# Optimization experiments

Hardware: AMD Instinct MI355X
Metric: run time of the kernel (lower is better)

## Reference

```python
import jax, jax.numpy as jnp
import numpy as np

LN_EPS = 1e-5


def _mlp(x, W1, b1, W2, b2, g, beta):
    # build_mlp_d: Linear -> ReLU -> Linear -> LayerNorm (mlp_layers=2, lay_norm=True)
    h = jax.nn.relu(x @ W1 + b1)
    h = h @ W2 + b2
    mu = jnp.mean(h, axis=-1, keepdims=True)
    var = jnp.var(h, axis=-1, keepdims=True)
    return (h - mu) * jax.lax.rsqrt(var + LN_EPS) * g + beta


def setup_inputs() -> dict:
    E, N, L, EIF = 524288, 65536, 128, 3
    key = jax.random.key(0)
    ks = iter(jax.random.split(key, 48))
    def rn(shape, s=1.0):
        return jax.random.normal(next(ks), shape, dtype=jnp.float32) * s
    inp = {}
    inp["edge_index"] = jax.random.randint(next(ks), (2, E), 0, N)
    inp["edge_dx_"] = rn((E, 3))
    inp["edge_attr"] = rn((E, EIF))
    for nm in ["vector_a", "vector_b", "vector_c",
               "senders_v_t_", "senders_v_tm1_", "senders_w_t_", "senders_w_tm1_",
               "senders_a_t_", "senders_alpha_t_",
               "receivers_v_t_", "receivers_v_tm1_", "receivers_w_t_", "receivers_w_tm1_",
               "receivers_a_t_", "receivers_alpha_t_"]:
        inp[nm] = rn((E, 3))
    inp["node_latent"] = rn((N, L))
    def mlp_params(pfx, din):
        inp[pfx + "_W1"] = rn((din, L), 0.05)
        inp[pfx + "_b1"] = jnp.zeros((L,), jnp.float32)
        inp[pfx + "_W2"] = rn((L, L), 0.05)
        inp[pfx + "_b2"] = jnp.zeros((L,), jnp.float32)
        inp[pfx + "_g"] = jnp.ones((L,), jnp.float32)
        inp[pfx + "_beta"] = jnp.zeros((L,), jnp.float32)
    mlp_params("fe", 18)        # edge_feat_encoder
    mlp_params("ee", 1 + EIF)   # edge_encoder
    mlp_params("ie", 3 * L)     # interaction_encoder
    return inp


def reference(edge_index, edge_dx_, edge_attr, vector_a, vector_b, vector_c,
              senders_v_t_, senders_v_tm1_, senders_w_t_, senders_w_tm1_,
              senders_a_t_, senders_alpha_t_,
              receivers_v_t_, receivers_v_tm1_, receivers_w_t_, receivers_w_tm1_,
              receivers_a_t_, receivers_alpha_t_,
              node_latent,
              fe_W1, fe_b1, fe_W2, fe_b2, fe_g, fe_beta,
              ee_W1, ee_b1, ee_W2, ee_b2, ee_g, ee_beta,
              ie_W1, ie_b1, ie_W2, ie_b2, ie_g, ie_beta):
    senders, receivers = edge_index[0], edge_index[1]
    basis = jnp.stack([vector_a, vector_b, vector_c], axis=1)  # [E,3,3]
    # Fuse the 12 small bmm projections into two batched einsums.
    s_stack = jnp.stack([senders_v_t_, senders_v_tm1_, senders_w_t_, senders_w_tm1_,
                         senders_a_t_, senders_alpha_t_], axis=1)   # [E,6,3]
    r_stack = jnp.stack([receivers_v_t_, receivers_v_tm1_, receivers_w_t_, receivers_w_tm1_,
                         receivers_a_t_, receivers_alpha_t_], axis=1)
    s_proj = jnp.einsum('eij,ekj->eki', basis, s_stack)  # [E,6,3]
    r_proj = jnp.einsum('eij,ekj->eki', basis, r_stack)
    # signs: -v_t, -v_tm1, -w_t, +w_tm1, -a_t, +alpha_t (receivers side)
    r_sign = jnp.array([-1.0, -1.0, -1.0, 1.0, -1.0, 1.0], jnp.float32)[None, :, None]
    E = s_proj.shape[0]
    senders_features = s_proj.reshape(E, 18)
    receivers_features = (r_proj * r_sign).reshape(E, 18)
    edge_dx_norm = jnp.linalg.norm(edge_dx_, axis=1, keepdims=True)  # [E,1]
    edge_latent = _mlp(jnp.concatenate([edge_dx_norm, edge_attr], axis=1),
                       ee_W1, ee_b1, ee_W2, ee_b2, ee_g, ee_beta)
    senders_latent = _mlp(senders_features, fe_W1, fe_b1, fe_W2, fe_b2, fe_g, fe_beta)
    receivers_latent = _mlp(receivers_features, fe_W1, fe_b1, fe_W2, fe_b2, fe_g, fe_beta)
    node_sum = node_latent[senders] + node_latent[receivers]  # [E,L]
    msg_input = jnp.concatenate([senders_latent + receivers_latent, node_sum, edge_latent], axis=1)
    return _mlp(msg_input, ie_W1, ie_b1, ie_W2, ie_b2, ie_g, ie_beta)
```

## Files before the change

### kernel.cpp

```cpp
#include <hip/hip_runtime.h>

typedef __attribute__((ext_vector_type(4))) float fx4;
typedef __attribute__((ext_vector_type(8))) unsigned short u16x8;
typedef __attribute__((ext_vector_type(8))) __bf16 bf16x8;

static __device__ __forceinline__ unsigned short f2bf(float f) {
  unsigned int u = __builtin_bit_cast(unsigned int, f);
  u += 0x7fffu + ((u >> 16) & 1u);
  return (unsigned short)(u >> 16);
}
static __device__ __forceinline__ fx4 mfma16(u16x8 a, u16x8 b, fx4 c) {
  return __builtin_amdgcn_mfma_f32_16x16x32_bf16(
      __builtin_bit_cast(bf16x8, a), __builtin_bit_cast(bf16x8, b), c, 0, 0, 0);
}

static __device__ __forceinline__ int swz128(int row, int col) {
  return row * 128 + (col ^ ((row & 7) << 3));
}
static __device__ __forceinline__ int swz32(int row, int col) {
  return row * 32 + (col ^ (((row >> 1) & 3) << 3));
}

#define WT_FE1 0
#define WT_FE2 4096
#define WT_EE1 20480
#define WT_EE2 24576
#define WT_A   40960
#define WT_B   57344
#define WT_C   73728
#define WT_IE2 90112
#define WT_TOTAL 106496

__global__ void prep_weights(const float* __restrict__ feW1, const float* __restrict__ feW2,
                             const float* __restrict__ eeW1, const float* __restrict__ eeW2,
                             const float* __restrict__ ieW1, const float* __restrict__ ieW2,
                             unsigned short* __restrict__ wt) {
  int i = blockIdx.x * 256 + threadIdx.x;
  if (i >= WT_TOTAL) return;
  int base, n, k, kpad;
  float val;
  if (i < WT_FE2)      { base = WT_FE1; n = i >> 5; k = i & 31; kpad = 32;
                         val = (k < 18) ? feW1[k * 128 + n] : 0.f; }
  else if (i < WT_EE1) { base = WT_FE2; int j = i - WT_FE2; n = j >> 7; k = j & 127; kpad = 128;
                         val = feW2[k * 128 + n]; }
  else if (i < WT_EE2) { base = WT_EE1; int j = i - WT_EE1; n = j >> 5; k = j & 31; kpad = 32;
                         val = (k < 4) ? eeW1[k * 128 + n] : 0.f; }
  else if (i < WT_A)   { base = WT_EE2; int j = i - WT_EE2; n = j >> 7; k = j & 127; kpad = 128;
                         val = eeW2[k * 128 + n]; }
  else if (i < WT_B)   { base = WT_A;   int j = i - WT_A;   n = j >> 7; k = j & 127; kpad = 128;
                         val = ieW1[k * 128 + n]; }
  else if (i < WT_C)   { base = WT_B;   int j = i - WT_B;   n = j >> 7; k = j & 127; kpad = 128;
                         val = ieW1[(128 + k) * 128 + n]; }
  else if (i < WT_IE2) { base = WT_C;   int j = i - WT_C;   n = j >> 7; k = j & 127; kpad = 128;
                         val = ieW1[(256 + k) * 128 + n]; }
  else                 { base = WT_IE2; int j = i - WT_IE2; n = j >> 7; k = j & 127; kpad = 128;
                         val = ieW2[k * 128 + n]; }
  int dst = (kpad == 32) ? base + n * 32 + (k ^ (((n >> 1) & 3) << 3))
                         : base + n * 128 + (k ^ ((n & 7) << 3));
  wt[dst] = f2bf(val);
}

template<int KPAD, int KT>
static __device__ __forceinline__ void gemm_lds(const unsigned short* As,
                                                const unsigned short* Ws,
                                                fx4* acc, int l16, int lgr) {
#pragma unroll
  for (int kk = 0; kk < KT; kk++) {
    const int k0 = kk * 32 + lgr * 8;
    u16x8 af = *(const u16x8*)(As + ((KPAD == 32) ? swz32(l16, k0) : swz128(l16, k0)));
#pragma unroll
    for (int nt = 0; nt < 8; nt++) {
      const int n = nt * 16 + l16;
      u16x8 bf = *(const u16x8*)(Ws + ((KPAD == 32) ? swz32(n, k0) : swz128(n, k0)));
      acc[nt] = mfma16(af, bf, acc[nt]);
    }
  }
}

static __device__ __forceinline__ void relu_store(fx4* acc, const float* __restrict__ bias,
                                                  unsigned short* dst, int l16, int lgr) {
#pragma unroll
  for (int nt = 0; nt < 8; nt++) {
    const int col = nt * 16 + l16;
    const float b = bias[col];
#pragma unroll
    for (int r = 0; r < 4; r++) {
      float v = acc[nt][r] + b;
      dst[swz128(lgr * 4 + r, col)] = f2bf(v > 0.f ? v : 0.f);
    }
  }
}

static __device__ __forceinline__ void ln_rows(fx4* acc, const float* __restrict__ bias, int l16) {
  float sum[4] = {0, 0, 0, 0}, sq[4] = {0, 0, 0, 0};
#pragma unroll
  for (int nt = 0; nt < 8; nt++) {
    const float b = bias[nt * 16 + l16];
#pragma unroll
    for (int r = 0; r < 4; r++) {
      float v = acc[nt][r] + b; acc[nt][r] = v;
      sum[r] += v; sq[r] += v * v;
    }
  }
#pragma unroll
  for (int r = 0; r < 4; r++) {
    float s_ = sum[r], q_ = sq[r];
#pragma unroll
    for (int m = 1; m < 16; m <<= 1) { s_ += __shfl_xor(s_, m, 64); q_ += __shfl_xor(q_, m, 64); }
    const float mu = s_ * (1.f / 128.f);
    const float rs = rsqrtf(q_ * (1.f / 128.f) - mu * mu + 1e-5f);
#pragma unroll
    for (int nt = 0; nt < 8; nt++) acc[nt][r] = (acc[nt][r] - mu) * rs;
  }
}

struct ParamsFE {
  const float* basis[3];
  const float* sv[6]; const float* rv[6];
  const float* b1; const float* b2; const float* g; const float* be;
  const unsigned short* wt;
  unsigned short* msg;
  int ntiles;
};

__global__ __launch_bounds__(512) void fe_kernel(ParamsFE p) {
  extern __shared__ unsigned short lds[];
  const int tid = threadIdx.x;
  const int wave = tid >> 6, lane = tid & 63;
  const int l16 = lane & 15, lgr = lane >> 4;
#pragma unroll
  for (int i = tid * 8; i < 20480; i += 4096)
    *(u16x8*)(lds + i) = *(const u16x8*)(p.wt + WT_FE1 + i);
  const unsigned short* W1 = lds;
  const unsigned short* W2 = lds + 4096;
  unsigned short* h1 = lds + 20480 + wave * 2560;
  unsigned short* feat = h1 + 2048;
  __syncthreads();
#pragma unroll
  for (int j = 0; j < 4; j++) { int c = 18 + lgr * 4 + j; if (c < 32) feat[swz32(l16, c)] = 0; }
  const fx4 z4 = {0.f, 0.f, 0.f, 0.f};

  for (int t = blockIdx.x; t < p.ntiles; t += gridDim.x) {
    const int e0 = t * 128 + wave * 16;
    const size_t e = (size_t)(e0 + l16);
    float bx[3][3];
#pragma unroll
    for (int i = 0; i < 3; i++) {
      const float* bp = p.basis[i] + 3 * e;
      bx[i][0] = bp[0]; bx[i][1] = bp[1]; bx[i][2] = bp[2];
    }
    fx4 latS[8];
#pragma unroll
    for (int side = 0; side < 2; side++) {
      const bool isR = (side == 1);
#pragma unroll
      for (int k = 0; k < 6; k++) {
        if ((k & 3) == lgr) {
          const float* vp = (isR ? p.rv[k] : p.sv[k]) + 3 * e;
          const float v0 = vp[0], v1 = vp[1], v2 = vp[2];
          const float sgn = (isR && k != 3 && k != 5) ? -1.f : 1.f;
#pragma unroll
          for (int i = 0; i < 3; i++) {
            float d = (bx[i][0] * v0 + bx[i][1] * v1 + bx[i][2] * v2) * sgn;
            feat[swz32(l16, k * 3 + i)] = f2bf(d);
          }
        }
      }
      fx4 acc[8];
#pragma unroll
      for (int b = 0; b < 8; b++) acc[b] = z4;
      gemm_lds<32, 1>(feat, W1, acc, l16, lgr);
      relu_store(acc, p.b1, h1, l16, lgr);
#pragma unroll
      for (int b = 0; b < 8; b++) acc[b] = z4;
      gemm_lds<128, 4>(h1, W2, acc, l16, lgr);
      ln_rows(acc, p.b2, l16);
      if (!isR) {
#pragma unroll
        for (int nt = 0; nt < 8; nt++) {
          const int col = nt * 16 + l16;
          const float gg = p.g[col], bb = p.be[col];
#pragma unroll
          for (int r = 0; r < 4; r++) latS[nt][r] = acc[nt][r] * gg + bb;
        }
      } else {
#pragma unroll
        for (int nt = 0; nt < 8; nt++) {
          const int col = nt * 16 + l16;
          const float gg = p.g[col], bb = p.be[col];
#pragma unroll
          for (int r = 0; r < 4; r++)
            p.msg[(size_t)(e0 + lgr * 4 + r) * 256 + col] =
                f2bf(latS[nt][r] + acc[nt][r] * gg + bb);
        }
      }
    }
  }
}

struct ParamsEE {
  const float* dx; const float* attr;
  const float* b1; const float* b2; const float* g; const float* be;
  const unsigned short* wt;
  unsigned short* msg;
  int ntiles;
};

__global__ __launch_bounds__(512) void ee_kernel(ParamsEE p) {
  extern __shared__ unsigned short lds[];
  const int tid = threadIdx.x;
  const int wave = tid >> 6, lane = tid & 63;
  const int l16 = lane & 15, lgr = lane >> 4;
#pragma unroll
  for (int i = tid * 8; i < 20480; i += 4096)
    *(u16x8*)(lds + i) = *(const u16x8*)(p.wt + WT_EE1 + i);
  const unsigned short* W1 = lds;
  const unsigned short* W2 = lds + 4096;
  unsigned short* h1 = lds + 20480 + wave * 2560;
  unsigned short* feat = h1 + 2048;
  __syncthreads();
#pragma unroll
  for (int j = 0; j < 7; j++) feat[swz32(l16, 4 + lgr * 7 + j)] = 0;
  const fx4 z4 = {0.f, 0.f, 0.f, 0.f};

  for (int t = blockIdx.x; t < p.ntiles; t += gridDim.x) {
    const int e0 = t * 128 + wave * 16;
    const size_t e = (size_t)(e0 + l16);
    if (lgr == 0) {
      float d0 = p.dx[3 * e], d1 = p.dx[3 * e + 1], d2 = p.dx[3 * e + 2];
      feat[swz32(l16, 0)] = f2bf(sqrtf(d0 * d0 + d1 * d1 + d2 * d2));
    } else {
      feat[swz32(l16, lgr)] = f2bf(p.attr[3 * e + (lgr - 1)]);
    }
    fx4 acc[8];
#pragma unroll
    for (int b = 0; b < 8; b++) acc[b] = z4;
    gemm_lds<32, 1>(feat, W1, acc, l16, lgr);
    relu_store(acc, p.b1, h1, l16, lgr);
#pragma unroll
    for (int b = 0; b < 8; b++) acc[b] = z4;
    gemm_lds<128, 4>(h1, W2, acc, l16, lgr);
    ln_rows(acc, p.b2, l16);
#pragma unroll
    for (int nt = 0; nt < 8; nt++) {
      const int col = nt * 16 + l16;
      const float gg = p.g[col], bb = p.be[col];
#pragma unroll
      for (int r = 0; r < 4; r++)
        p.msg[(size_t)(e0 + lgr * 4 + r) * 256 + 128 + col] =
            f2bf(acc[nt][r] * gg + bb);
    }
  }
}

struct ParamsIE {
  const int* eidx;
  const float* nl;
  const float* b1; const float* b2; const float* g; const float* be;
  const unsigned short* wt;
  const unsigned short* msg;
  float* out;
  int E; int ntiles;
};

__global__ __launch_bounds__(512) void ie_kernel(ParamsIE p) {
  extern __shared__ unsigned short dyn[];
  const int tid = threadIdx.x;
  const int wave = tid >> 6, lane = tid & 63;
  const int l16 = lane & 15, lgr = lane >> 4;
#pragma unroll
  for (int i = tid * 8; i < 49152; i += 4096)
    *(u16x8*)(dyn + i) = *(const u16x8*)(p.wt + WT_A + i);
  const unsigned short* WA = dyn;
  const unsigned short* WB = dyn + 16384;
  const unsigned short* WC = dyn + 32768;
  unsigned short* h1 = dyn + 49152 + wave * 2048;
  __syncthreads();
  const fx4 z4 = {0.f, 0.f, 0.f, 0.f};

  for (int t = blockIdx.x; t < p.ntiles; t += gridDim.x) {
    const int e0 = t * 128 + wave * 16;
    const size_t e = (size_t)(e0 + l16);
    const int sidx = p.eidx[e];
    const int ridx = p.eidx[(size_t)p.E + e];
    const unsigned short* mrow = p.msg + e * 256;
    const float* ns = p.nl + (size_t)sidx * 128;
    const float* nr = p.nl + (size_t)ridx * 128;
    fx4 acc[8];
#pragma unroll
    for (int b = 0; b < 8; b++) acc[b] = z4;
#pragma unroll
    for (int c = 0; c < 4; c++) {
      const int k0 = c * 32 + lgr * 8;
      fx4 a0 = *(const fx4*)(ns + k0), a1 = *(const fx4*)(ns + k0 + 4);
      fx4 b0 = *(const fx4*)(nr + k0), b1 = *(const fx4*)(nr + k0 + 4);
      u16x8 af;
#pragma unroll
      for (int j = 0; j < 4; j++) { af[j] = f2bf(a0[j] + b0[j]); af[4 + j] = f2bf(a1[j] + b1[j]); }
#pragma unroll
      for (int nt = 0; nt < 8; nt++) {
        u16x8 bf = *(const u16x8*)(WB + swz128(nt * 16 + l16, k0));
        acc[nt] = mfma16(af, bf, acc[nt]);
      }
    }
#pragma unroll
    for (int c = 0; c < 4; c++) {
      const int k0 = c * 32 + lgr * 8;
      u16x8 af = *(const u16x8*)(mrow + k0);
#pragma unroll
      for (int nt = 0; nt < 8; nt++) {
        u16x8 bf = *(const u16x8*)(WA + swz128(nt * 16 + l16, k0));
        acc[nt] = mfma16(af, bf, acc[nt]);
      }
    }
#pragma unroll
    for (int c = 0; c < 4; c++) {
      const int k0 = c * 32 + lgr * 8;
      u16x8 af = *(const u16x8*)(mrow + 128 + k0);
#pragma unroll
      for (int nt = 0; nt < 8; nt++) {
        u16x8 bf = *(const u16x8*)(WC + swz128(nt * 16 + l16, k0));
        acc[nt] = mfma16(af, bf, acc[nt]);
      }
    }
    relu_store(acc, p.b1, h1, l16, lgr);
#pragma unroll
    for (int b = 0; b < 8; b++) acc[b] = z4;
    gemm_lds<128, 4>(h1, p.wt + WT_IE2, acc, l16, lgr);
    ln_rows(acc, p.b2, l16);
#pragma unroll
    for (int nt = 0; nt < 8; nt++) {
      const int col = nt * 16 + l16;
      const float gg = p.g[col], bb = p.be[col];
#pragma unroll
      for (int r = 0; r < 4; r++)
        p.out[(size_t)(e0 + lgr * 4 + r) * 128 + col] = acc[nt][r] * gg + bb;
    }
  }
}

extern "C" void kernel_launch(void* const* d_in, const int* in_sizes, int n_in,
                              void* d_out, int out_size, void* d_ws, size_t ws_size,
                              hipStream_t stream) {
  (void)n_in; (void)out_size;
  const int E = in_sizes[1] / 3;
  unsigned short* wt = reinterpret_cast<unsigned short*>(d_ws);
  if (ws_size < (size_t)WT_TOTAL * sizeof(unsigned short)) return;

  prep_weights<<<(WT_TOTAL + 255) / 256, 256, 0, stream>>>(
      (const float*)d_in[19], (const float*)d_in[21],
      (const float*)d_in[25], (const float*)d_in[27],
      (const float*)d_in[31], (const float*)d_in[33], wt);

  unsigned short* msg = (unsigned short*)d_out;

  hipFuncSetAttribute((const void*)fe_kernel,
                      hipFuncAttributeMaxDynamicSharedMemorySize, 81920);
  hipFuncSetAttribute((const void*)ee_kernel,
                      hipFuncAttributeMaxDynamicSharedMemorySize, 81920);
  hipFuncSetAttribute((const void*)ie_kernel,
                      hipFuncAttributeMaxDynamicSharedMemorySize, 131072);

  ParamsFE pf;
  for (int i = 0; i < 3; i++) pf.basis[i] = (const float*)d_in[3 + i];
  for (int k = 0; k < 6; k++) { pf.sv[k] = (const float*)d_in[6 + k]; pf.rv[k] = (const float*)d_in[12 + k]; }
  pf.b1 = (const float*)d_in[20]; pf.b2 = (const float*)d_in[22];
  pf.g  = (const float*)d_in[23]; pf.be = (const float*)d_in[24];
  pf.wt = wt; pf.msg = msg; pf.ntiles = E / 128;
  fe_kernel<<<512, 512, 81920, stream>>>(pf);

  ParamsEE pe;
  pe.dx = (const float*)d_in[1]; pe.attr = (const float*)d_in[2];
  pe.b1 = (const float*)d_in[26]; pe.b2 = (const float*)d_in[28];
  pe.g  = (const float*)d_in[29]; pe.be = (const float*)d_in[30];
  pe.wt = wt; pe.msg = msg; pe.ntiles = E / 128;
  ee_kernel<<<512, 512, 81920, stream>>>(pe);

  ParamsIE pi;
  pi.eidx = (const int*)d_in[0];
  pi.nl = (const float*)d_in[18];
  pi.b1 = (const float*)d_in[32]; pi.b2 = (const float*)d_in[34];
  pi.g  = (const float*)d_in[35]; pi.be = (const float*)d_in[36];
  pi.wt = wt; pi.msg = msg; pi.out = (float*)d_out;
  pi.E = E; pi.ntiles = E / 128;
  ie_kernel<<<256, 512, 131072, stream>>>(pi);
}
```

Baseline: 549.5 us.

## Merge FE and EE kernels into one launch and widen IE blocks to 12 waves

The separate FE and EE encoder kernels become one launch whose blocks are split by index: the first 512 run the FE body and the rest run the EE body. This lets the two independent stages run concurrently and removes one launch boundary. The IE kernel moves to 768 threads per block with per-wave 16-edge tiles and a larger LDS allocation, so more waves share each copy of the weights. The larger LDS and register footprint per block may limit occupancy.

```diff
diff --git a/kernel.cpp b/kernel.cpp
--- a/kernel.cpp
+++ b/kernel.cpp
@@ -118,19 +118,21 @@
   const float* basis[3];
   const float* sv[6]; const float* rv[6];
   const float* b1; const float* b2; const float* g; const float* be;
-  const unsigned short* wt;
-  unsigned short* msg;
-  int ntiles;
 };
-
-__global__ __launch_bounds__(512) void fe_kernel(ParamsFE p) {
-  extern __shared__ unsigned short lds[];
+struct ParamsEE {
+  const float* dx; const float* attr;
+  const float* b1; const float* b2; const float* g; const float* be;
+};
+
+static __device__ __forceinline__ void fe_body(const ParamsFE& p, unsigned short* lds,
+                                               const unsigned short* wt, unsigned short* msg,
+                                               int bid, int nblocks, int ntiles) {
   const int tid = threadIdx.x;
   const int wave = tid >> 6, lane = tid & 63;
   const int l16 = lane & 15, lgr = lane >> 4;
 #pragma unroll
   for (int i = tid * 8; i < 20480; i += 4096)
-    *(u16x8*)(lds + i) = *(const u16x8*)(p.wt + WT_FE1 + i);
+    *(u16x8*)(lds + i) = *(const u16x8*)(wt + WT_FE1 + i);
   const unsigned short* W1 = lds;
   const unsigned short* W2 = lds + 4096;
   unsigned short* h1 = lds + 20480 + wave * 2560;
@@ -140,7 +142,7 @@
   for (int j = 0; j < 4; j++) { int c = 18 + lgr * 4 + j; if (c < 32) feat[swz32(l16, c)] = 0; }
   const fx4 z4 = {0.f, 0.f, 0.f, 0.f};
 
-  for (int t = blockIdx.x; t < p.ntiles; t += gridDim.x) {
+  for (int t = bid; t < ntiles; t += nblocks) {
     const int e0 = t * 128 + wave * 16;
     const size_t e = (size_t)(e0 + l16);
     float bx[3][3];
@@ -190,7 +192,7 @@
           const float gg = p.g[col], bb = p.be[col];
 #pragma unroll
           for (int r = 0; r < 4; r++)
-            p.msg[(size_t)(e0 + lgr * 4 + r) * 256 + col] =
+            msg[(size_t)(e0 + lgr * 4 + r) * 256 + col] =
                 f2bf(latS[nt][r] + acc[nt][r] * gg + bb);
         }
       }
@@ -198,22 +200,15 @@
   }
 }
 
-struct ParamsEE {
-  const float* dx; const float* attr;
-  const float* b1; const float* b2; const float* g; const float* be;
-  const unsigned short* wt;
-  unsigned short* msg;
-  int ntiles;
-};
-
-__global__ __launch_bounds__(512) void ee_kernel(ParamsEE p) {
-  extern __shared__ unsigned short lds[];
+static __device__ __forceinline__ void ee_body(const ParamsEE& p, unsigned short* lds,
+                                               const unsigned short* wt, unsigned short* msg,
+                                               int bid, int nblocks, int ntiles) {
   const int tid = threadIdx.x;
   const int wave = tid >> 6, lane = tid & 63;
   const int l16 = lane & 15, lgr = lane >> 4;
 #pragma unroll
   for (int i = tid * 8; i < 20480; i += 4096)
-    *(u16x8*)(lds + i) = *(const u16x8*)(p.wt + WT_EE1 + i);
+    *(u16x8*)(lds + i) = *(const u16x8*)(wt + WT_EE1 + i);
   const unsigned short* W1 = lds;
   const unsigned short* W2 = lds + 4096;
   unsigned short* h1 = lds + 20480 + wave * 2560;
@@ -223,7 +218,7 @@
   for (int j = 0; j < 7; j++) feat[swz32(l16, 4 + lgr * 7 + j)] = 0;
   const fx4 z4 = {0.f, 0.f, 0.f, 0.f};
 
-  for (int t = blockIdx.x; t < p.ntiles; t += gridDim.x) {
+  for (int t = bid; t < ntiles; t += nblocks) {
     const int e0 = t * 128 + wave * 16;
     const size_t e = (size_t)(e0 + l16);
     if (lgr == 0) {
@@ -247,10 +242,21 @@
       const float gg = p.g[col], bb = p.be[col];
 #pragma unroll
       for (int r = 0; r < 4; r++)
-        p.msg[(size_t)(e0 + lgr * 4 + r) * 256 + 128 + col] =
+        msg[(size_t)(e0 + lgr * 4 + r) * 256 + 128 + col] =
             f2bf(acc[nt][r] * gg + bb);
     }
   }
+}
+
+__global__ __launch_bounds__(512) void feee_kernel(ParamsFE pf, ParamsEE pe,
+                                                   const unsigned short* wt,
+                                                   unsigned short* msg,
+                                                   int nfe, int ntiles) {
+  extern __shared__ unsigned short lds[];
+  if ((int)blockIdx.x < nfe)
+    fe_body(pf, lds, wt, msg, blockIdx.x, nfe, ntiles);
+  else
+    ee_body(pe, lds, wt, msg, blockIdx.x - nfe, gridDim.x - nfe, ntiles);
 }
 
 struct ParamsIE {
@@ -260,16 +266,15 @@
   const unsigned short* wt;
   const unsigned short* msg;
   float* out;
-  int E; int ntiles;
+  int E; int nt16;
 };
 
-__global__ __launch_bounds__(512) void ie_kernel(ParamsIE p) {
+__global__ __launch_bounds__(768) void ie_kernel(ParamsIE p) {
   extern __shared__ unsigned short dyn[];
   const int tid = threadIdx.x;
   const int wave = tid >> 6, lane = tid & 63;
   const int l16 = lane & 15, lgr = lane >> 4;
-#pragma unroll
-  for (int i = tid * 8; i < 49152; i += 4096)
+  for (int i = tid * 8; i < 49152; i += 6144)
     *(u16x8*)(dyn + i) = *(const u16x8*)(p.wt + WT_A + i);
   const unsigned short* WA = dyn;
   const unsigned short* WB = dyn + 16384;
@@ -278,8 +283,10 @@
   __syncthreads();
   const fx4 z4 = {0.f, 0.f, 0.f, 0.f};
 
-  for (int t = blockIdx.x; t < p.ntiles; t += gridDim.x) {
-    const int e0 = t * 128 + wave * 16;
+  const int gw = blockIdx.x * 12 + wave;
+  const int gstride = gridDim.x * 12;
+  for (int t = gw; t < p.nt16; t += gstride) {
+    const int e0 = t * 16;
     const size_t e = (size_t)(e0 + l16);
     const int sidx = p.eidx[e];
     const int ridx = p.eidx[(size_t)p.E + e];
@@ -354,27 +361,23 @@
 
   unsigned short* msg = (unsigned short*)d_out;
 
-  hipFuncSetAttribute((const void*)fe_kernel,
-                      hipFuncAttributeMaxDynamicSharedMemorySize, 81920);
-  hipFuncSetAttribute((const void*)ee_kernel,
+  hipFuncSetAttribute((const void*)feee_kernel,
                       hipFuncAttributeMaxDynamicSharedMemorySize, 81920);
   hipFuncSetAttribute((const void*)ie_kernel,
-                      hipFuncAttributeMaxDynamicSharedMemorySize, 131072);
+                      hipFuncAttributeMaxDynamicSharedMemorySize, 147456);
 
   ParamsFE pf;
   for (int i = 0; i < 3; i++) pf.basis[i] = (const float*)d_in[3 + i];
   for (int k = 0; k < 6; k++) { pf.sv[k] = (const float*)d_in[6 + k]; pf.rv[k] = (const float*)d_in[12 + k]; }
   pf.b1 = (const float*)d_in[20]; pf.b2 = (const float*)d_in[22];
   pf.g  = (const float*)d_in[23]; pf.be = (const float*)d_in[24];
-  pf.wt = wt; pf.msg = msg; pf.ntiles = E / 128;
-  fe_kernel<<<512, 512, 81920, stream>>>(pf);
 
   ParamsEE pe;
   pe.dx = (const float*)d_in[1]; pe.attr = (const float*)d_in[2];
   pe.b1 = (const float*)d_in[26]; pe.b2 = (const float*)d_in[28];
   pe.g  = (const float*)d_in[29]; pe.be = (const float*)d_in[30];
-  pe.wt = wt; pe.msg = msg; pe.ntiles = E / 128;
-  ee_kernel<<<512, 512, 81920, stream>>>(pe);
+
+  feee_kernel<<<1024, 512, 81920, stream>>>(pf, pe, wt, msg, 512, E / 128);
 
   ParamsIE pi;
   pi.eidx = (const int*)d_in[0];
@@ -382,6 +385,6 @@
   pi.b1 = (const float*)d_in[32]; pi.b2 = (const float*)d_in[34];
   pi.g  = (const float*)d_in[35]; pi.be = (const float*)d_in[36];
   pi.wt = wt; pi.msg = msg; pi.out = (float*)d_out;
-  pi.E = E; pi.ntiles = E / 128;
-  ie_kernel<<<256, 512, 131072, stream>>>(pi);
-}
+  pi.E = E; pi.nt16 = E / 16;
+  ie_kernel<<<256, 768, 147456, stream>>>(pi);
+}
```

Result: slower. 638.0 us (+16.1%).
